# Kernel tuning notes

Measured on AMD Instinct MI355X. Metric: run time of the kernel, lower is better.

The kernel has to match this reference:

```python
import jax, jax.numpy as jnp
import numpy as np
import math

K = 128
H = 8

def setup_inputs() -> dict:
    key = jax.random.key(0)
    ks = jax.random.split(key, 6)
    x = jax.random.normal(ks[0], (4, 2048, K), dtype=jnp.float32)
    # torch nn.Linear weights have shape (out_features, in_features)
    s = 1.0 / math.sqrt(K)
    Wq = jax.random.uniform(ks[1], (K * H, K), minval=-s, maxval=s, dtype=jnp.float32)
    Wk = jax.random.uniform(ks[2], (K * H, K), minval=-s, maxval=s, dtype=jnp.float32)
    Wv = jax.random.uniform(ks[3], (K * H, K), minval=-s, maxval=s, dtype=jnp.float32)
    so = 1.0 / math.sqrt(K * H)
    Wo = jax.random.uniform(ks[4], (K, K * H), minval=-so, maxval=so, dtype=jnp.float32)
    bo = jax.random.uniform(ks[5], (K,), minval=-so, maxval=so, dtype=jnp.float32)
    return {"x": x, "Wq": Wq, "Wk": Wk, "Wv": Wv, "Wo": Wo, "bo": bo}

def reference(x, Wq, Wk, Wv, Wo, bo):
    b, c, k = x.shape
    h = H
    # Linear(k, k*h, bias=False): x @ W.T, then view (b, c, h, k)
    q = (x @ Wq.T).reshape(b, c, h, k)
    kk = (x @ Wk.T).reshape(b, c, h, k)
    v = (x @ Wv.T).reshape(b, c, h, k)
    # Original: einsum('bchk,bihe->bhci') sums k and e INDEPENDENTLY
    # (quirk of the source). Equivalent factored form (same math, cheaper):
    dot = jnp.einsum('bch,bih->bhci', q.sum(-1), kk.sum(-1)) / math.sqrt(k)
    attn = jax.nn.softmax(dot, axis=-1)                      # (b, h, c, c)
    # einsum('bchd,bdce->bhce') on dot(b,h,c,i), values(b,i,h,e):
    out = jnp.einsum('bhti,bihe->bthe', attn, v)             # (b, c, h, k)
    # final: einsum('bthe,khe->btk', out, Wo.view(k, h, k)) + bias
    y = jnp.einsum('bthe,khe->btk', out, Wo.reshape(k, h, k)) + bo
    return y
```

## Files before the change

kernel.cpp:

```cpp
#include <hip/hip_runtime.h>
#include <math.h>

#define NB 4
#define NC 2048
#define NH 8
#define NK 128
#define NG 255

#define A2SCALE (1.4426950408889634f * 0.08838834764831845f)

typedef __attribute__((ext_vector_type(8))) short bf16x8;
typedef __attribute__((ext_vector_type(4))) float f32x4;

#define OFF_MM  0
#define OFF_W2  8192
#define OFF_QS  139264
#define OFF_KS  204800
#define OFF_XB  270336
#define OFF_PN  4464640

__device__ static inline float exp2_hw(float x) {
#if __has_builtin(__builtin_amdgcn_exp2f)
    return __builtin_amdgcn_exp2f(x);
#else
    float r;
    asm volatile("v_exp_f32 %0, %1\n\ts_nop 1" : "=v"(r) : "v"(x));
    return r;
#endif
}

__device__ static inline unsigned cvtpk(float lo, float hi) {
    unsigned r;
    asm("v_cvt_pk_bf16_f32 %0, %1, %2" : "=v"(r) : "v"(lo), "v"(hi));
    return r;
}

__device__ static inline bf16x8 pack8(float4 a, float4 b) {
    union { unsigned u[4]; bf16x8 v; } r;
    r.u[0] = cvtpk(a.x, a.y);
    r.u[1] = cvtpk(a.z, a.w);
    r.u[2] = cvtpk(b.x, b.y);
    r.u[3] = cvtpk(b.z, b.w);
    return r.v;
}

__device__ static inline bf16x8 pexp8s(float4 ka, float4 kb, float a, float negM,
                                       float& z) {
    float e0 = exp2_hw(fmaf(a, ka.x, negM));
    float e1 = exp2_hw(fmaf(a, ka.y, negM));
    float e2 = exp2_hw(fmaf(a, ka.z, negM));
    float e3 = exp2_hw(fmaf(a, ka.w, negM));
    float e4 = exp2_hw(fmaf(a, kb.x, negM));
    float e5 = exp2_hw(fmaf(a, kb.y, negM));
    float e6 = exp2_hw(fmaf(a, kb.z, negM));
    float e7 = exp2_hw(fmaf(a, kb.w, negM));
    z += ((e0 + e1) + (e2 + e3)) + ((e4 + e5) + (e6 + e7));
    union { unsigned u[4]; bf16x8 v; } r;
    r.u[0] = cvtpk(e0, e1);
    r.u[1] = cvtpk(e2, e3);
    r.u[2] = cvtpk(e4, e5);
    r.u[3] = cvtpk(e6, e7);
    return r.v;
}

__global__ __launch_bounds__(256) void k_prep1(const float* __restrict__ Wq,
                                               const float* __restrict__ Wk,
                                               const float* __restrict__ Wv,
                                               const float* __restrict__ Wo,
                                               float* __restrict__ wspart,
                                               float* __restrict__ W2) {
    int blk = blockIdx.x;
    int tid = threadIdx.x;
    __shared__ float sh[256];
    if (blk < 64) {
        int which = blk >> 5, h = (blk >> 2) & 7, eq = blk & 3;
        const float* W = which ? Wk : Wq;
        int m = tid & 127, part = tid >> 7;
        const float* base = W + (h * 128 + eq * 32 + part * 16) * 128 + m;
        float s = 0.f;
#pragma unroll
        for (int e = 0; e < 16; ++e) s += base[e * 128];
        if (part) sh[m] = s;
        __syncthreads();
        if (!part) wspart[eq * 2048 + which * 1024 + h * 128 + m] = s + sh[m];
    } else {
        int idx = blk - 64;
        int h = idx >> 6;
        int kl = tid >> 7;
        int kk = (idx & 63) * 2 + kl;
        int m = tid & 127;
        float* wo_s = sh;
        wo_s[kl * 128 + m] = Wo[kk * 1024 + h * 128 + m];
        __syncthreads();
        const float* base = Wv + (h * 128) * 128 + m;
        const float* wrow = &wo_s[kl * 128];
        float s = 0.f;
#pragma unroll 4
        for (int e = 0; e < 128; ++e) s += base[e * 128] * wrow[e];
        W2[(h * 128 + kk) * 128 + m] = s;
    }
}

__global__ __launch_bounds__(256) void k_prep2(const float* __restrict__ x,
                                               const float* __restrict__ wspart,
                                               float* __restrict__ qs,
                                               float* __restrict__ ks,
                                               unsigned short* __restrict__ xbf) {
    __shared__ float xs[32][129];
    __shared__ float wsum[2048];
    int tid = threadIdx.x;
    int blk = blockIdx.x;
    for (int j = tid; j < 2048; j += 256)
        wsum[j] = wspart[j] + wspart[2048 + j] + wspart[4096 + j] + wspart[6144 + j];
    int row0 = blk * 32;
    for (int j = tid; j < 32 * 128; j += 256) {
        int r = j >> 7, m = j & 127;
        xs[r][m] = x[(size_t)(row0 + r) * 128 + m];
    }
    __syncthreads();
#pragma unroll
    for (int jj = 0; jj < 2; ++jj) {
        int o = tid + 256 * jj;
        int r = o & 31;
        int q = o >> 5;
        int which = q >> 3, h = q & 7;
        const float* wrow = &wsum[which * 1024 + h * 128];
        const float* xrow = &xs[r][0];
        float s = 0.f;
#pragma unroll 4
        for (int m = 0; m < 128; ++m) s += xrow[m] * wrow[m];
        int row = row0 + r, b = row >> 11, t = row & 2047;
        float* dst = which ? ks : qs;
        dst[(b * 8 + h) * 2048 + t] = s;
    }
    {
        int b = row0 >> 11;
        int ig = (row0 >> 5) & 63;
        unsigned short* xb = xbf + (size_t)(b * 64 + ig) * 4096;
#pragma unroll
        for (int qq = 0; qq < 2; ++qq) {
            int q = tid + qq * 256;
            int nt = q >> 6, lane = q & 63;
            int l4 = lane >> 4, m = nt * 16 + (lane & 15);
            int ib = l4 * 8;
            union { unsigned u[4]; uint4 v; } pk;
            pk.u[0] = cvtpk(xs[ib + 0][m], xs[ib + 1][m]);
            pk.u[1] = cvtpk(xs[ib + 2][m], xs[ib + 3][m]);
            pk.u[2] = cvtpk(xs[ib + 4][m], xs[ib + 5][m]);
            pk.u[3] = cvtpk(xs[ib + 6][m], xs[ib + 7][m]);
            *(uint4*)&xb[(size_t)nt * 512 + lane * 8] = pk.v;
        }
    }
}

__global__ __launch_bounds__(256, 2) void k_c(const float* __restrict__ qs,
                                              const float* __restrict__ ks,
                                              const unsigned short* __restrict__ xbf,
                                              float* __restrict__ pC,
                                              float* __restrict__ pz,
                                              float* __restrict__ mm) {
    int L = blockIdx.x;
    int xcd = L & 7, s = L >> 3;
    int bh = xcd * 4 + (s >> 4);
    int rem = s & 15;
    int gt = rem >> 2, sl = rem & 3;
    int b = bh >> 3;
    int tid = threadIdx.x;
    int lane = tid & 63, wid = tid >> 6;
    int l15 = lane & 15, l4 = lane >> 4;

    __shared__ float kss[2048];
    __shared__ __align__(16) unsigned short u_l[3][4096];
    __shared__ float red[8];

    for (int j = tid; j < 512; j += 256)
        ((float4*)kss)[j] = ((const float4*)(qs + bh * 2048))[j];
    __syncthreads();
    float mn = 1e30f, mx = -1e30f;
    {
        const float4* ka = (const float4*)kss;
#pragma unroll
        for (int jj = 0; jj < 2; ++jj) {
            float4 v = ka[tid + jj * 256];
            mn = fminf(mn, fminf(fminf(v.x, v.y), fminf(v.z, v.w)));
            mx = fmaxf(mx, fmaxf(fmaxf(v.x, v.y), fmaxf(v.z, v.w)));
        }
#pragma unroll
        for (int off = 32; off; off >>= 1) {
            mn = fminf(mn, __shfl_xor(mn, off));
            mx = fmaxf(mx, __shfl_xor(mx, off));
        }
        if (!lane) { red[wid] = mn; red[4 + wid] = mx; }
    }
    __syncthreads();
    mn = fminf(fminf(red[0], red[1]), fminf(red[2], red[3]));
    mx = fmaxf(fmaxf(red[4], red[5]), fmaxf(red[6], red[7]));
    float amin = mn * A2SCALE;
    float hstep = fmaxf((mx * A2SCALE - amin), 1e-6f) * (1.f / (NG - 1));
    if (tid == 0) { mm[bh * 2] = amin; mm[bh * 2 + 1] = hstep; }
    __syncthreads();

    for (int j = tid; j < 512; j += 256)
        ((float4*)kss)[j] = ((const float4*)(ks + bh * 2048))[j];
    __syncthreads();
    mn = 1e30f; mx = -1e30f;
    {
        const float4* ka = (const float4*)kss;
#pragma unroll
        for (int jj = 0; jj < 2; ++jj) {
            float4 v = ka[tid + jj * 256];
            mn = fminf(mn, fminf(fminf(v.x, v.y), fminf(v.z, v.w)));
            mx = fmaxf(mx, fmaxf(fmaxf(v.x, v.y), fmaxf(v.z, v.w)));
        }
#pragma unroll
        for (int off = 32; off; off >>= 1) {
            mn = fminf(mn, __shfl_xor(mn, off));
            mx = fmaxf(mx, __shfl_xor(mx, off));
        }
        if (!lane) { red[wid] = mn; red[4 + wid] = mx; }
    }
    __syncthreads();
    mn = fminf(fminf(red[0], red[1]), fminf(red[2], red[3]));
    mx = fmaxf(fmaxf(red[4], red[5]), fmaxf(red[6], red[7]));

    int grow = gt * 64 + wid * 16 + l15;
    float a = fmaf((float)grow, hstep, amin);
    float negM = -(a > 0.f ? a * mx : a * mn);
    float zacc = 0.f;

    const unsigned short* gxb = xbf + (size_t)b * 262144 + (size_t)sl * 65536;

    f32x4 acc[8];
#pragma unroll
    for (int n = 0; n < 8; ++n) acc[n] = (f32x4)0.f;

#define DMA(cnv, buf) do {                                                     \
    const unsigned short* src_ = gxb + (size_t)(cnv) * 4096;                   \
    _Pragma("unroll")                                                          \
    for (int q_ = 0; q_ < 2; ++q_) {                                           \
        int seg_ = q_ * 4 + wid;                                               \
        __builtin_amdgcn_global_load_lds(                                      \
            (const __attribute__((address_space(1))) unsigned int*)(src_ + seg_ * 512 + lane * 8), \
            (__attribute__((address_space(3))) unsigned int*)(&u_l[buf][seg_ * 512]),              \
            16, 0, 0);                                                         \
    }                                                                          \
} while (0)

    DMA(0, 0);
    DMA(1, 1);
    for (int cn = 0; cn < 15; ++cn) {
        int cur = cn % 3;
        int ib = sl * 512 + cn * 32;
        float4 ka = *(const float4*)&kss[ib + l4 * 8];
        float4 kb = *(const float4*)&kss[ib + l4 * 8 + 4];
        bf16x8 pf = pexp8s(ka, kb, a, negM, zacc);

        asm volatile("s_waitcnt vmcnt(2)" ::: "memory");
        __builtin_amdgcn_sched_barrier(0);
        __builtin_amdgcn_s_barrier();
        __builtin_amdgcn_sched_barrier(0);
        if (cn + 2 <= 15) DMA(cn + 2, (cn + 2) % 3);
        __builtin_amdgcn_sched_barrier(0);

        __builtin_amdgcn_s_setprio(1);
#pragma unroll
        for (int n = 0; n < 8; ++n) {
            bf16x8 uf = *(const bf16x8*)&u_l[cur][n * 512 + lane * 8];
            acc[n] = __builtin_amdgcn_mfma_f32_16x16x32_bf16(pf, uf, acc[n], 0, 0, 0);
        }
        __builtin_amdgcn_s_setprio(0);
    }
    {
        int ib = sl * 512 + 15 * 32;
        float4 ka = *(const float4*)&kss[ib + l4 * 8];
        float4 kb = *(const float4*)&kss[ib + l4 * 8 + 4];
        bf16x8 pf = pexp8s(ka, kb, a, negM, zacc);
        asm volatile("s_waitcnt vmcnt(0)" ::: "memory");
        __builtin_amdgcn_sched_barrier(0);
        __builtin_amdgcn_s_barrier();
        __builtin_amdgcn_sched_barrier(0);
#pragma unroll
        for (int n = 0; n < 8; ++n) {
            bf16x8 uf = *(const bf16x8*)&u_l[0][n * 512 + lane * 8];
            acc[n] = __builtin_amdgcn_mfma_f32_16x16x32_bf16(pf, uf, acc[n], 0, 0, 0);
        }
    }
#undef DMA

    zacc += __shfl_xor(zacc, 16);
    zacc += __shfl_xor(zacc, 32);
    if (l4 == 0 && grow < NG)
        pz[(bh * 4 + sl) * NG + grow] = zacc;

#pragma unroll
    for (int r = 0; r < 4; ++r) {
        int g = gt * 64 + wid * 16 + l4 * 4 + r;
        if (g < NG) {
            float* row = pC + ((size_t)(bh * 4 + sl) * NG + g) * 128;
#pragma unroll
            for (int n = 0; n < 8; ++n)
                row[n * 16 + l15] = acc[n][r];
        }
    }
}

__global__ __launch_bounds__(256) void k_n(float* __restrict__ pC,
                                           const float* __restrict__ pz,
                                           const float* __restrict__ W2) {
    int L = blockIdx.x;
    int bh = L >> 2, gt = L & 3;
    int h = bh & 7;
    int tid = threadIdx.x;
    int lane = tid & 63, wid = tid >> 6;
    int wr = wid >> 1, wc = wid & 1;
    int l15 = lane & 15, l4 = lane >> 4;

    const float* w2h = W2 + h * 16384;
    const size_t slo = (size_t)NG * 128;
    const size_t cb = (size_t)(bh * 4) * NG * 128;

    f32x4 acc[2][4];
#pragma unroll
    for (int mg = 0; mg < 2; ++mg)
#pragma unroll
        for (int nt = 0; nt < 4; ++nt) acc[mg][nt] = (f32x4)0.f;

#pragma unroll
    for (int kq = 0; kq < 4; ++kq) {
        bf16x8 af[2], bfr[4];
#pragma unroll
        for (int mg = 0; mg < 2; ++mg) {
            int g = gt * 64 + wr * 32 + mg * 16 + l15;
            size_t base = cb + (size_t)g * 128 + kq * 32 + l4 * 8;
            float4 sa = *(const float4*)&pC[base];
            float4 sb = *(const float4*)&pC[base + 4];
#pragma unroll
            for (int sl = 1; sl < 4; ++sl) {
                float4 ta = *(const float4*)&pC[base + sl * slo];
                float4 tb = *(const float4*)&pC[base + sl * slo + 4];
                sa.x += ta.x; sa.y += ta.y; sa.z += ta.z; sa.w += ta.w;
                sb.x += tb.x; sb.y += tb.y; sb.z += tb.z; sb.w += tb.w;
            }
            af[mg] = pack8(sa, sb);
        }
#pragma unroll
        for (int nt = 0; nt < 4; ++nt) {
            int kk = wc * 64 + nt * 16 + l15;
            const float* src = w2h + kk * 128 + kq * 32 + l4 * 8;
            bfr[nt] = pack8(*(const float4*)src, *(const float4*)(src + 4));
        }
#pragma unroll
        for (int mg = 0; mg < 2; ++mg)
#pragma unroll
            for (int nt = 0; nt < 4; ++nt)
                acc[mg][nt] = __builtin_amdgcn_mfma_f32_16x16x32_bf16(
                    af[mg], bfr[nt], acc[mg][nt], 0, 0, 0);
    }

    __syncthreads();

#pragma unroll
    for (int mg = 0; mg < 2; ++mg) {
#pragma unroll
        for (int r = 0; r < 4; ++r) {
            int g = gt * 64 + wr * 32 + mg * 16 + l4 * 4 + r;
            if (g < NG) {
                float z = pz[(bh * 4 + 0) * NG + g] + pz[(bh * 4 + 1) * NG + g] +
                          pz[(bh * 4 + 2) * NG + g] + pz[(bh * 4 + 3) * NG + g];
                float zinv = 1.f / z;
                float* row = pC + cb + (size_t)g * 128;
#pragma unroll
                for (int nt = 0; nt < 4; ++nt)
                    row[wc * 64 + nt * 16 + l15] = acc[mg][nt][r] * zinv;
            }
        }
    }
}

__global__ __launch_bounds__(256) void k_eval(const float* __restrict__ qs,
                                              const float* __restrict__ tablef,
                                              const float* __restrict__ mm,
                                              const float* __restrict__ bo,
                                              float* __restrict__ y) {
    int blk = blockIdx.x;
    int b = blk >> 7;
    int t = (blk & 127) * 16 + (threadIdx.x >> 4);
    int kk0 = (threadIdx.x & 15) * 8;

    float acc[8];
#pragma unroll
    for (int j = 0; j < 8; ++j) acc[j] = bo[kk0 + j];

#pragma unroll
    for (int h = 0; h < 8; ++h) {
        int bh = b * 8 + h;
        float a = qs[bh * 2048 + t] * A2SCALE;
        float amin = mm[bh * 2], hs = mm[bh * 2 + 1];
        float p = (a - amin) / hs;
        int g1 = (int)p;
        g1 = g1 < 1 ? 1 : (g1 > NG - 3 ? NG - 3 : g1);
        float u = p - (float)g1;
        float um1 = u - 1.f, um2 = u - 2.f, up1 = u + 1.f;
        float w0 = -u * um1 * um2 * (1.f / 6.f);
        float w1 = up1 * um1 * um2 * 0.5f;
        float w2 = -up1 * u * um2 * 0.5f;
        float w3 = up1 * u * um1 * (1.f / 6.f);
        const float* base = tablef + ((size_t)(bh * 4) * NG + (g1 - 1)) * 128 + kk0;
#pragma unroll
        for (int v = 0; v < 2; ++v) {
            float4 r0 = *(const float4*)(base + v * 4);
            float4 r1 = *(const float4*)(base + 128 + v * 4);
            float4 r2 = *(const float4*)(base + 256 + v * 4);
            float4 r3 = *(const float4*)(base + 384 + v * 4);
            acc[v * 4 + 0] += w0 * r0.x + w1 * r1.x + w2 * r2.x + w3 * r3.x;
            acc[v * 4 + 1] += w0 * r0.y + w1 * r1.y + w2 * r2.y + w3 * r3.y;
            acc[v * 4 + 2] += w0 * r0.z + w1 * r1.z + w2 * r2.z + w3 * r3.z;
            acc[v * 4 + 3] += w0 * r0.w + w1 * r1.w + w2 * r2.w + w3 * r3.w;
        }
    }
    float* yp = y + ((size_t)b * 2048 + t) * 128 + kk0;
    *(float4*)yp = make_float4(acc[0], acc[1], acc[2], acc[3]);
    *(float4*)(yp + 4) = make_float4(acc[4], acc[5], acc[6], acc[7]);
}

extern "C" void kernel_launch(void* const* d_in, const int* in_sizes, int n_in,
                              void* d_out, int out_size, void* d_ws, size_t ws_size,
                              hipStream_t stream) {
    const float* x  = (const float*)d_in[0];
    const float* Wq = (const float*)d_in[1];
    const float* Wk = (const float*)d_in[2];
    const float* Wv = (const float*)d_in[3];
    const float* Wo = (const float*)d_in[4];
    const float* bo = (const float*)d_in[5];
    float* y  = (float*)d_out;
    float* ws = (float*)d_ws;
    (void)in_sizes; (void)n_in; (void)out_size; (void)ws_size;

    unsigned short* xbf = (unsigned short*)(ws + OFF_XB);
    float* pC = ws + OFF_PN;
    float* pz = y;
    float* mm = ws + OFF_MM;

    k_prep1<<<576, 256, 0, stream>>>(Wq, Wk, Wv, Wo, ws, ws + OFF_W2);
    k_prep2<<<256, 256, 0, stream>>>(x, ws, ws + OFF_QS, ws + OFF_KS, xbf);
    k_c<<<512, 256, 0, stream>>>(ws + OFF_QS, ws + OFF_KS, xbf, pC, pz, mm);
    k_n<<<128, 256, 0, stream>>>(pC, pz, ws + OFF_W2);
    k_eval<<<512, 256, 0, stream>>>(ws + OFF_QS, pC, mm, bo, y);
}
```

Before: 68.13 us.

## Compute q/k min-max via atomics in prep2 and preload whole x slice in k_c

The per-(b,h) min/max of q and k sums now comes from order-preserving unsigned atomics in k_prep2, so k_c no longer loads and reduces the full q and k vectors. k_c also loads its entire 128 KB bf16 x slice into LDS up front with one wait and barrier, replacing the triple-buffered DMA pipeline with its per-chunk barriers. The cost is 128 KB of LDS per block, which drops occupancy to one block per CU and removes overlap between the loads and the MFMA work. k_eval recomputes the step size from the encoded min/max instead of reading a stored value.

Result: slower. 73.99 us (+8.6%).

```diff
diff --git a/kernel.cpp b/kernel.cpp
--- a/kernel.cpp
+++ b/kernel.cpp
@@ -12,11 +12,11 @@
 typedef __attribute__((ext_vector_type(8))) short bf16x8;
 typedef __attribute__((ext_vector_type(4))) float f32x4;
 
-#define OFF_MM  0
 #define OFF_W2  8192
 #define OFF_QS  139264
 #define OFF_KS  204800
 #define OFF_XB  270336
+#define OFF_MMU 794624
 #define OFF_PN  4464640
 
 __device__ static inline float exp2_hw(float x) {
@@ -42,6 +42,14 @@
     r.u[2] = cvtpk(b.x, b.y);
     r.u[3] = cvtpk(b.z, b.w);
     return r.v;
+}
+
+__device__ static inline unsigned fenc(float f) {
+    unsigned b = __float_as_uint(f);
+    return (b & 0x80000000u) ? ~b : (b | 0x80000000u);
+}
+__device__ static inline float fdec(unsigned k) {
+    return __uint_as_float((k & 0x80000000u) ? (k & 0x7FFFFFFFu) : ~k);
 }
 
 __device__ static inline bf16x8 pexp8s(float4 ka, float4 kb, float a, float negM,
@@ -68,7 +76,8 @@
                                                const float* __restrict__ Wv,
                                                const float* __restrict__ Wo,
                                                float* __restrict__ wspart,
-                                               float* __restrict__ W2) {
+                                               float* __restrict__ W2,
+                                               unsigned* __restrict__ mmu) {
     int blk = blockIdx.x;
     int tid = threadIdx.x;
     __shared__ float sh[256];
@@ -83,6 +92,8 @@
         if (part) sh[m] = s;
         __syncthreads();
         if (!part) wspart[eq * 2048 + which * 1024 + h * 128 + m] = s + sh[m];
+        if (blk == 0 && tid < 128)
+            mmu[tid] = (tid & 1) ? 0u : 0xFFFFFFFFu;
     } else {
         int idx = blk - 64;
         int h = idx >> 6;
@@ -105,7 +116,8 @@
                                                const float* __restrict__ wspart,
                                                float* __restrict__ qs,
                                                float* __restrict__ ks,
-                                               unsigned short* __restrict__ xbf) {
+                                               unsigned short* __restrict__ xbf,
+                                               unsigned* __restrict__ mmu) {
     __shared__ float xs[32][129];
     __shared__ float wsum[2048];
     int tid = threadIdx.x;
@@ -132,6 +144,17 @@
         int row = row0 + r, b = row >> 11, t = row & 2047;
         float* dst = which ? ks : qs;
         dst[(b * 8 + h) * 2048 + t] = s;
+        float gmn = s, gmx = s;
+#pragma unroll
+        for (int off = 1; off <= 16; off <<= 1) {
+            gmn = fminf(gmn, __shfl_xor(gmn, off));
+            gmx = fmaxf(gmx, __shfl_xor(gmx, off));
+        }
+        if (r == 0) {
+            unsigned* mb = &mmu[(b * 8 + h) * 4 + which * 2];
+            atomicMin(&mb[0], fenc(gmn));
+            atomicMax(&mb[1], fenc(gmx));
+        }
     }
     {
         int b = row0 >> 11;
@@ -153,12 +176,11 @@
     }
 }
 
-__global__ __launch_bounds__(256, 2) void k_c(const float* __restrict__ qs,
-                                              const float* __restrict__ ks,
+__global__ __launch_bounds__(256, 1) void k_c(const float* __restrict__ ks,
                                               const unsigned short* __restrict__ xbf,
+                                              const unsigned* __restrict__ mmu,
                                               float* __restrict__ pC,
-                                              float* __restrict__ pz,
-                                              float* __restrict__ mm) {
+                                              float* __restrict__ pz) {
     int L = blockIdx.x;
     int xcd = L & 7, s = L >> 3;
     int bh = xcd * 4 + (s >> 4);
@@ -169,123 +191,53 @@
     int lane = tid & 63, wid = tid >> 6;
     int l15 = lane & 15, l4 = lane >> 4;
 
-    __shared__ float kss[2048];
-    __shared__ __align__(16) unsigned short u_l[3][4096];
-    __shared__ float red[8];
-
-    for (int j = tid; j < 512; j += 256)
-        ((float4*)kss)[j] = ((const float4*)(qs + bh * 2048))[j];
-    __syncthreads();
-    float mn = 1e30f, mx = -1e30f;
+    __shared__ __align__(16) unsigned short x_l[65536];
+    __shared__ float ks_s[512];
+
+    float amin = fdec(mmu[bh * 4]) * A2SCALE;
+    float amax = fdec(mmu[bh * 4 + 1]) * A2SCALE;
+    float hstep = fmaxf(amax - amin, 1e-6f) * (1.f / (NG - 1));
+    float kmn = fdec(mmu[bh * 4 + 2]);
+    float kmx = fdec(mmu[bh * 4 + 3]);
+
+    if (tid < 128)
+        ((float4*)ks_s)[tid] = ((const float4*)(ks + bh * 2048 + sl * 512))[tid];
     {
-        const float4* ka = (const float4*)kss;
-#pragma unroll
-        for (int jj = 0; jj < 2; ++jj) {
-            float4 v = ka[tid + jj * 256];
-            mn = fminf(mn, fminf(fminf(v.x, v.y), fminf(v.z, v.w)));
-            mx = fmaxf(mx, fmaxf(fmaxf(v.x, v.y), fmaxf(v.z, v.w)));
-        }
-#pragma unroll
-        for (int off = 32; off; off >>= 1) {
-            mn = fminf(mn, __shfl_xor(mn, off));
-            mx = fmaxf(mx, __shfl_xor(mx, off));
-        }
-        if (!lane) { red[wid] = mn; red[4 + wid] = mx; }
-    }
-    __syncthreads();
-    mn = fminf(fminf(red[0], red[1]), fminf(red[2], red[3]));
-    mx = fmaxf(fmaxf(red[4], red[5]), fmaxf(red[6], red[7]));
-    float amin = mn * A2SCALE;
-    float hstep = fmaxf((mx * A2SCALE - amin), 1e-6f) * (1.f / (NG - 1));
-    if (tid == 0) { mm[bh * 2] = amin; mm[bh * 2 + 1] = hstep; }
-    __syncthreads();
-
-    for (int j = tid; j < 512; j += 256)
-        ((float4*)kss)[j] = ((const float4*)(ks + bh * 2048))[j];
-    __syncthreads();
-    mn = 1e30f; mx = -1e30f;
-    {
-        const float4* ka = (const float4*)kss;
-#pragma unroll
-        for (int jj = 0; jj < 2; ++jj) {
-            float4 v = ka[tid + jj * 256];
-            mn = fminf(mn, fminf(fminf(v.x, v.y), fminf(v.z, v.w)));
-            mx = fmaxf(mx, fmaxf(fmaxf(v.x, v.y), fmaxf(v.z, v.w)));
-        }
-#pragma unroll
-        for (int off = 32; off; off >>= 1) {
-            mn = fminf(mn, __shfl_xor(mn, off));
-            mx = fmaxf(mx, __shfl_xor(mx, off));
-        }
-        if (!lane) { red[wid] = mn; red[4 + wid] = mx; }
-    }
-    __syncthreads();
-    mn = fminf(fminf(red[0], red[1]), fminf(red[2], red[3]));
-    mx = fmaxf(fmaxf(red[4], red[5]), fmaxf(red[6], red[7]));
+        const unsigned short* gxb = xbf + (size_t)b * 262144 + (size_t)sl * 65536;
+#pragma unroll 4
+        for (int q = 0; q < 32; ++q) {
+            int S = q * 4 + wid;
+            __builtin_amdgcn_global_load_lds(
+                (const __attribute__((address_space(1))) unsigned int*)(gxb + S * 512 + lane * 8),
+                (__attribute__((address_space(3))) unsigned int*)(x_l + S * 512),
+                16, 0, 0);
+        }
+    }
 
     int grow = gt * 64 + wid * 16 + l15;
     float a = fmaf((float)grow, hstep, amin);
-    float negM = -(a > 0.f ? a * mx : a * mn);
+    float negM = -(a > 0.f ? a * kmx : a * kmn);
     float zacc = 0.f;
 
-    const unsigned short* gxb = xbf + (size_t)b * 262144 + (size_t)sl * 65536;
-
     f32x4 acc[8];
 #pragma unroll
     for (int n = 0; n < 8; ++n) acc[n] = (f32x4)0.f;
 
-#define DMA(cnv, buf) do {                                                     \
-    const unsigned short* src_ = gxb + (size_t)(cnv) * 4096;                   \
-    _Pragma("unroll")                                                          \
-    for (int q_ = 0; q_ < 2; ++q_) {                                           \
-        int seg_ = q_ * 4 + wid;                                               \
-        __builtin_amdgcn_global_load_lds(                                      \
-            (const __attribute__((address_space(1))) unsigned int*)(src_ + seg_ * 512 + lane * 8), \
-            (__attribute__((address_space(3))) unsigned int*)(&u_l[buf][seg_ * 512]),              \
-            16, 0, 0);                                                         \
-    }                                                                          \
-} while (0)
-
-    DMA(0, 0);
-    DMA(1, 1);
-    for (int cn = 0; cn < 15; ++cn) {
-        int cur = cn % 3;
-        int ib = sl * 512 + cn * 32;
-        float4 ka = *(const float4*)&kss[ib + l4 * 8];
-        float4 kb = *(const float4*)&kss[ib + l4 * 8 + 4];
+    __syncthreads();
+
+    for (int cn = 0; cn < 16; ++cn) {
+        float4 ka = *(const float4*)&ks_s[cn * 32 + l4 * 8];
+        float4 kb = *(const float4*)&ks_s[cn * 32 + l4 * 8 + 4];
         bf16x8 pf = pexp8s(ka, kb, a, negM, zacc);
-
-        asm volatile("s_waitcnt vmcnt(2)" ::: "memory");
-        __builtin_amdgcn_sched_barrier(0);
-        __builtin_amdgcn_s_barrier();
-        __builtin_amdgcn_sched_barrier(0);
-        if (cn + 2 <= 15) DMA(cn + 2, (cn + 2) % 3);
-        __builtin_amdgcn_sched_barrier(0);
-
+        const unsigned short* xc = &x_l[cn * 4096];
         __builtin_amdgcn_s_setprio(1);
 #pragma unroll
         for (int n = 0; n < 8; ++n) {
-            bf16x8 uf = *(const bf16x8*)&u_l[cur][n * 512 + lane * 8];
+            bf16x8 uf = *(const bf16x8*)&xc[n * 512 + lane * 8];
             acc[n] = __builtin_amdgcn_mfma_f32_16x16x32_bf16(pf, uf, acc[n], 0, 0, 0);
         }
         __builtin_amdgcn_s_setprio(0);
     }
-    {
-        int ib = sl * 512 + 15 * 32;
-        float4 ka = *(const float4*)&kss[ib + l4 * 8];
-        float4 kb = *(const float4*)&kss[ib + l4 * 8 + 4];
-        bf16x8 pf = pexp8s(ka, kb, a, negM, zacc);
-        asm volatile("s_waitcnt vmcnt(0)" ::: "memory");
-        __builtin_amdgcn_sched_barrier(0);
-        __builtin_amdgcn_s_barrier();
-        __builtin_amdgcn_sched_barrier(0);
-#pragma unroll
-        for (int n = 0; n < 8; ++n) {
-            bf16x8 uf = *(const bf16x8*)&u_l[0][n * 512 + lane * 8];
-            acc[n] = __builtin_amdgcn_mfma_f32_16x16x32_bf16(pf, uf, acc[n], 0, 0, 0);
-        }
-    }
-#undef DMA
 
     zacc += __shfl_xor(zacc, 16);
     zacc += __shfl_xor(zacc, 32);
@@ -379,7 +331,7 @@
 
 __global__ __launch_bounds__(256) void k_eval(const float* __restrict__ qs,
                                               const float* __restrict__ tablef,
-                                              const float* __restrict__ mm,
+                                              const unsigned* __restrict__ mmu,
                                               const float* __restrict__ bo,
                                               float* __restrict__ y) {
     int blk = blockIdx.x;
@@ -395,7 +347,9 @@
     for (int h = 0; h < 8; ++h) {
         int bh = b * 8 + h;
         float a = qs[bh * 2048 + t] * A2SCALE;
-        float amin = mm[bh * 2], hs = mm[bh * 2 + 1];
+        float amin = fdec(mmu[bh * 4]) * A2SCALE;
+        float amax = fdec(mmu[bh * 4 + 1]) * A2SCALE;
+        float hs = fmaxf(amax - amin, 1e-6f) * (1.f / (NG - 1));
         float p = (a - amin) / hs;
         int g1 = (int)p;
         g1 = g1 < 1 ? 1 : (g1 > NG - 3 ? NG - 3 : g1);
@@ -437,13 +391,13 @@
     (void)in_sizes; (void)n_in; (void)out_size; (void)ws_size;
 
     unsigned short* xbf = (unsigned short*)(ws + OFF_XB);
+    unsigned* mmu = (unsigned*)(ws + OFF_MMU);
     float* pC = ws + OFF_PN;
     float* pz = y;
-    float* mm = ws + OFF_MM;
-
-    k_prep1<<<576, 256, 0, stream>>>(Wq, Wk, Wv, Wo, ws, ws + OFF_W2);
-    k_prep2<<<256, 256, 0, stream>>>(x, ws, ws + OFF_QS, ws + OFF_KS, xbf);
-    k_c<<<512, 256, 0, stream>>>(ws + OFF_QS, ws + OFF_KS, xbf, pC, pz, mm);
+
+    k_prep1<<<576, 256, 0, stream>>>(Wq, Wk, Wv, Wo, ws, ws + OFF_W2, mmu);
+    k_prep2<<<256, 256, 0, stream>>>(x, ws, ws + OFF_QS, ws + OFF_KS, xbf, mmu);
+    k_c<<<512, 256, 0, stream>>>(ws + OFF_KS, xbf, mmu, pC, pz);
     k_n<<<128, 256, 0, stream>>>(pC, pz, ws + OFF_W2);
-    k_eval<<<512, 256, 0, stream>>>(ws + OFF_QS, pC, mm, bo, y);
-}
+    k_eval<<<512, 256, 0, stream>>>(ws + OFF_QS, pC, mmu, bo, y);
+}
```
